# Optimization experiments

Measured on AMD Instinct MI355X. Metric: run time of the kernel, lower is better.

Reference implementation:

```python
import jax, jax.numpy as jnp
import numpy as np

B, S, E, M = 128, 196, 768, 768

def setup_inputs() -> dict:
    key = jax.random.key(0)
    k1, k2, k3, k4, k5 = jax.random.split(key, 5)
    sent_emb = jax.random.normal(k1, (B, S, E), dtype=jnp.float32)
    # valid event spans: start in [0, S-6), end = start + len, len in [1,5]
    starts = jax.random.randint(k2, (B, 2), 0, S - 6)
    lens = jax.random.randint(k3, (B, 2), 1, 6)
    ends = starts + lens
    batch_e = jnp.stack([starts[:, 0], ends[:, 0], starts[:, 1], ends[:, 1]], axis=1).astype(jnp.int64)
    mlp_w = jax.random.normal(k4, (M, 2 * E), dtype=jnp.float32) * 0.02
    mlp_b = jnp.zeros((M,), dtype=jnp.float32)
    fk_w = jax.random.normal(k5, (M, S * E), dtype=jnp.float32) * 0.005
    fk_b = jnp.zeros((M,), dtype=jnp.float32)
    return {"sent_emb": sent_emb, "batch_e": batch_e, "mlp_w": mlp_w,
            "mlp_b": mlp_b, "fk_w": fk_w, "fk_b": fk_b, "batch_size": B}

def reference(sent_emb, batch_e, mlp_w, mlp_b, fk_w, fk_b, batch_size):
    b, s, e = sent_emb.shape
    # sent_process: flatten each sentence's [S,E] embeddings into one row [S*E]
    sent_emb_cat = sent_emb.reshape(b, s * e)  # [B, S*E]
    # extract_event: mean-pool over the two variable-length spans (vectorized via masks)
    pos = jnp.arange(s)  # [S]
    m1 = ((pos >= batch_e[:, 0:1]) & (pos < batch_e[:, 1:2])).astype(sent_emb.dtype)  # [B,S]
    m2 = ((pos >= batch_e[:, 2:3]) & (pos < batch_e[:, 3:4])).astype(sent_emb.dtype)
    e1 = jnp.einsum('bs,bse->be', m1, sent_emb) / jnp.sum(m1, axis=1, keepdims=True)
    e2 = jnp.einsum('bs,bse->be', m2, sent_emb) / jnp.sum(m2, axis=1, keepdims=True)
    event_pair = jnp.concatenate([e1, e2], axis=1)  # [B, 2E]
    pred = 0.9 * (event_pair @ mlp_w.T + mlp_b) + 0.1 * (sent_emb_cat @ fk_w.T + fk_b)
    return pred
```

## Files before the change

kernel.cpp:

```cpp
#include <hip/hip_runtime.h>
#include <hip/hip_bf16.h>

#define B_ 128
#define S_ 196
#define E_ 768
#define M_ 768
#define KTOT (S_*E_)
#define BK 256
#define SS_TOTAL (KTOT/BK)
#define KSPLIT 32
#define BN 48
#define MTN (M_/BN)
#define PITCH 528
#define ZC 4

typedef __bf16 bf16x8 __attribute__((ext_vector_type(8)));
typedef __bf16 bf16x4 __attribute__((ext_vector_type(4)));
typedef float  f32x4  __attribute__((ext_vector_type(4)));

__device__ inline bf16x8 cvt8(const float* __restrict__ p) {
    float4 a = *(const float4*)p;
    float4 b = *(const float4*)(p + 4);
    bf16x8 r;
    r[0] = (__bf16)a.x; r[1] = (__bf16)a.y; r[2] = (__bf16)a.z; r[3] = (__bf16)a.w;
    r[4] = (__bf16)b.x; r[5] = (__bf16)b.y; r[6] = (__bf16)b.z; r[7] = (__bf16)b.w;
    return r;
}

__device__ inline void barrier_nodrain() {
    asm volatile("s_waitcnt lgkmcnt(0)" ::: "memory");
    __builtin_amdgcn_s_barrier();
}

__global__ void prep(const float* __restrict__ mlp_b,
                     const float* __restrict__ fk_b,
                     const float* __restrict__ A,
                     const int* __restrict__ BE, int be_stride,
                     float* __restrict__ out,
                     float* __restrict__ EP,
                     __bf16* __restrict__ Apk) {
    const int bid = blockIdx.x;
    if (bid < 384) {
        int i = bid * 256 + threadIdx.x;
        int m = i % M_;
        out[i] = 0.9f * mlp_b[m] + 0.1f * fk_b[m];
    } else if (bid < 512) {
        int b = bid - 384;
        int s1 = BE[(b*4 + 0) * be_stride];
        int e1 = BE[(b*4 + 1) * be_stride];
        int s2 = BE[(b*4 + 2) * be_stride];
        int e2 = BE[(b*4 + 3) * be_stride];
        float inv1 = 1.0f / (float)(e1 - s1);
        float inv2 = 1.0f / (float)(e2 - s2);
        for (int c = threadIdx.x; c < E_; c += 256) {
            float sum1 = 0.f, sum2 = 0.f;
            for (int s = s1; s < e1; ++s) sum1 += A[((size_t)b * S_ + s) * E_ + c];
            for (int s = s2; s < e2; ++s) sum2 += A[((size_t)b * S_ + s) * E_ + c];
            EP[b * (2*E_) + c]       = sum1 * inv1;
            EP[b * (2*E_) + E_ + c]  = sum2 * inv2;
        }
    } else {
        const int nchunk = SS_TOTAL * 8 * 8 * 64;
        for (int c = (bid - 512) * 256 + threadIdx.x; c < nchunk; c += 3072 * 256) {
            int lane = c & 63;
            int kf   = (c >> 6) & 7;
            int bt   = (c >> 9) & 7;
            int ss   = c >> 12;
            int b = bt * 16 + (lane & 15);
            int k = ss * BK + kf * 32 + (lane >> 4) * 8;
            *(bf16x8*)(Apk + (size_t)c * 8) = cvt8(A + (size_t)b * KTOT + k);
        }
    }
}


#define LOAD_A(AREG, sl)                                                      \
    _Pragma("unroll")                                                         \
    for (int kf = 0; kf < 8; ++kf)                                            \
        AREG[kf] = *(const bf16x8*)(abase + (size_t)(sl) * 32768 + kf * 512);

#define LOAD_W(sl)                                                            \
    _Pragma("unroll")                                                         \
    for (int i = 0; i < 6; ++i)                                               \
        w[i] = *(const float4*)(wbase + (size_t)i * KTOT + (size_t)(sl) * BK);

#define WRITE_W(buf)                                                          \
    _Pragma("unroll")                                                         \
    for (int i = 0; i < 6; ++i) {                                             \
        bf16x4 h;                                                             \
        h[0] = (__bf16)w[i].x; h[1] = (__bf16)w[i].y;                         \
        h[2] = (__bf16)w[i].z; h[3] = (__bf16)w[i].w;                         \
        *(bf16x4*)(&Wlds[buf][0] + wb + i * PITCH) = h;                       \
    }

#define COMPUTE(AREG, buf)                                                    \
    _Pragma("unroll")                                                         \
    for (int kf = 0; kf < 8; ++kf) {                                          \
        _Pragma("unroll")                                                     \
        for (int n = 0; n < 3; ++n) {                                         \
            bf16x8 wf = *(const bf16x8*)(&Wlds[buf][0] +                      \
                        (n * 16 + r16) * PITCH + kf * 64 + kg * 16);          \
            acc[n] = __builtin_amdgcn_mfma_f32_16x16x32_bf16(AREG[kf], wf,    \
                                                             acc[n], 0, 0, 0);\
        }                                                                     \
    }

__global__
__attribute__((amdgpu_flat_work_group_size(512, 512), amdgpu_waves_per_eu(4, 4)))
void fk_gemm(const __bf16* __restrict__ Apk,
             const float* __restrict__ W,
             float* __restrict__ partial) {
    __shared__ __align__(16) char Wlds[2][BN * PITCH];

    const int wg   = blockIdx.x;
    const int xcd  = wg & 7;
    const int slot = wg >> 3;
    const int kz   = (slot >> 4) * 8 + xcd;
    const int mt   = slot & 15;
    const int ss0 = (SS_TOTAL * kz) / KSPLIT;
    const int SSN = (SS_TOTAL * (kz + 1)) / KSPLIT - ss0;

    const int tid = threadIdx.x;
    const int wv  = tid >> 6;
    const int lane = tid & 63;
    const int r16 = lane & 15;
    const int kg  = lane >> 4;

    const float*  wbase = W + (size_t)(mt * BN + wv * 6) * KTOT
                            + (size_t)ss0 * BK + lane * 4;
    const int     wb    = (wv * 6) * PITCH + lane * 8;
    const __bf16* abase = Apk + ((size_t)ss0 * 8 + wv) * 4096 + lane * 8;

    f32x4 acc[3] = {};
    float4 w[6];
    bf16x8 aA[8], aB[8];

    LOAD_W(0)
    WRITE_W(0)
    LOAD_A(aA, 0)
    LOAD_W(1)
    barrier_nodrain();

    int sl = 0;
    for (; sl + 1 < SSN; sl += 2) {
        LOAD_A(aB, sl + 1)
        COMPUTE(aA, 0)
        WRITE_W(1)
        const bool more2 = (sl + 2 < SSN);
        if (more2) { LOAD_W(sl + 2) }
        barrier_nodrain();
        if (more2) { LOAD_A(aA, sl + 2) }
        COMPUTE(aB, 1)
        if (more2) {
            WRITE_W(0)
            if (sl + 3 < SSN) { LOAD_W(sl + 3) }
            barrier_nodrain();
        }
    }
    if (SSN & 1) {
        COMPUTE(aA, 0)
    }

    float* pz = partial + (size_t)kz * (B_ * M_);
#pragma unroll
    for (int n = 0; n < 3; ++n) {
        const int m = mt * BN + n * 16 + r16;
#pragma unroll
        for (int r = 0; r < 4; ++r) {
            const int b = wv * 16 + kg * 4 + r;
            pz[(size_t)b * M_ + m] = acc[n][r];
        }
    }
}

__global__ __launch_bounds__(256) void post(const float* __restrict__ pp,
                                            const float* __restrict__ EP,
                                            const float* __restrict__ Wm,
                                            float* __restrict__ out) {
    const int bid = blockIdx.x;
    if (bid < 1536) {
        int t = bid * 256 + threadIdx.x;
        int i = t % (B_ * M_);
        int zc = t / (B_ * M_);
        float s = 0.f;
#pragma unroll
        for (int z = zc * (KSPLIT / ZC); z < (zc + 1) * (KSPLIT / ZC); ++z)
            s += pp[(size_t)z * (B_ * M_) + i];
        atomicAdd(out + i, 0.1f * s);
    } else {
        const int wid   = ((bid - 1536) * 256 + threadIdx.x) >> 6;
        const int lane  = threadIdx.x & 63;
        const int bt    = wid & 7;
        const int mt    = wid >> 3;
        const int row16 = lane & 15;
        const int kgrp  = lane >> 4;
        const float* Arow = EP + (size_t)(bt*16 + row16) * (2*E_);
        const float* Brow = Wm + (size_t)(mt*16 + row16) * (2*E_);
        f32x4 acc = {};
        for (int k0 = 0; k0 < 2*E_; k0 += 32) {
            bf16x8 af = cvt8(Arow + k0 + kgrp*8);
            bf16x8 bv = cvt8(Brow + k0 + kgrp*8);
            acc = __builtin_amdgcn_mfma_f32_16x16x32_bf16(af, bv, acc, 0, 0, 0);
        }
        const int m = mt*16 + row16;
#pragma unroll
        for (int r = 0; r < 4; ++r) {
            const int b = bt*16 + kgrp*4 + r;
            atomicAdd(out + b * M_ + m, 0.9f * acc[r]);
        }
    }
}

extern "C" void kernel_launch(void* const* d_in, const int* in_sizes, int n_in,
                              void* d_out, int out_size, void* d_ws, size_t ws_size,
                              hipStream_t stream) {
    const float* se    = (const float*)d_in[0];
    const int*   be    = (const int*)  d_in[1];
    const float* mlp_w = (const float*)d_in[2];
    const float* mlp_b = (const float*)d_in[3];
    const float* fk_w  = (const float*)d_in[4];
    const float* fk_b  = (const float*)d_in[5];
    float* out = (float*)d_out;
    float* ep  = (float*)d_ws;
    float* pp  = ep + (size_t)B_ * 2 * E_;
    __bf16* apk = (__bf16*)(pp + (size_t)KSPLIT * B_ * M_);

    const int be_stride = (in_sizes[1] == B_ * 4 * 2) ? 2 : 1;

    prep<<<3584, 256, 0, stream>>>(mlp_b, fk_b, se, be, be_stride, out, ep, apk);
    fk_gemm<<<MTN * KSPLIT, 512, 0, stream>>>(apk, fk_w, pp);
    post<<<1632, 256, 0, stream>>>(pp, ep, mlp_w, out);
}
```

Baseline: 167.3 us.

## Restructure fk_gemm pipeline to prefetch W two slices ahead and single-buffer A

Reorganizes the main GEMM loop so each iteration prefetches the next pair of W slices into two register sets while computing both LDS buffers. The A fragment is loaded immediately before each compute instead of being double-buffered in registers. This reduces A register pressure and gives W loads a full pair of iterations of latency hiding. The cost is exposed A global-load latency right before the MFMAs, plus two barriers per pair instead of interleaved single barriers.

Measured after the change: 177.1 us. +5.9%, slower.

```diff
diff --git a/kernel.cpp b/kernel.cpp
--- a/kernel.cpp
+++ b/kernel.cpp
@@ -74,33 +74,40 @@
 }
 
 
-#define LOAD_A(AREG, sl)                                                      \
+#define LOAD_A(sl)                                                            \
     _Pragma("unroll")                                                         \
     for (int kf = 0; kf < 8; ++kf)                                            \
-        AREG[kf] = *(const bf16x8*)(abase + (size_t)(sl) * 32768 + kf * 512);
-
-#define LOAD_W(sl)                                                            \
+        aA[kf] = *(const bf16x8*)(abase + (size_t)(sl) * 32768 + kf * 512);
+
+#define LOAD_PAIR(sl)                                                         \
+    _Pragma("unroll")                                                         \
+    for (int i = 0; i < 6; ++i) {                                             \
+        w0[i] = *(const float4*)(wbase + (size_t)i * KTOT + (size_t)(sl) * BK);\
+        w1[i] = *(const float4*)(wbase + (size_t)i * KTOT + (size_t)(sl) * BK + BK);\
+    }
+
+#define LOAD_ONE(WREG, sl)                                                    \
     _Pragma("unroll")                                                         \
     for (int i = 0; i < 6; ++i)                                               \
-        w[i] = *(const float4*)(wbase + (size_t)i * KTOT + (size_t)(sl) * BK);
-
-#define WRITE_W(buf)                                                          \
+        WREG[i] = *(const float4*)(wbase + (size_t)i * KTOT + (size_t)(sl) * BK);
+
+#define WRITE_W(WREG, buf)                                                    \
     _Pragma("unroll")                                                         \
     for (int i = 0; i < 6; ++i) {                                             \
         bf16x4 h;                                                             \
-        h[0] = (__bf16)w[i].x; h[1] = (__bf16)w[i].y;                         \
-        h[2] = (__bf16)w[i].z; h[3] = (__bf16)w[i].w;                         \
+        h[0] = (__bf16)WREG[i].x; h[1] = (__bf16)WREG[i].y;                   \
+        h[2] = (__bf16)WREG[i].z; h[3] = (__bf16)WREG[i].w;                   \
         *(bf16x4*)(&Wlds[buf][0] + wb + i * PITCH) = h;                       \
     }
 
-#define COMPUTE(AREG, buf)                                                    \
+#define COMPUTE(buf)                                                          \
     _Pragma("unroll")                                                         \
     for (int kf = 0; kf < 8; ++kf) {                                          \
         _Pragma("unroll")                                                     \
         for (int n = 0; n < 3; ++n) {                                         \
             bf16x8 wf = *(const bf16x8*)(&Wlds[buf][0] +                      \
                         (n * 16 + r16) * PITCH + kf * 64 + kg * 16);          \
-            acc[n] = __builtin_amdgcn_mfma_f32_16x16x32_bf16(AREG[kf], wf,    \
+            acc[n] = __builtin_amdgcn_mfma_f32_16x16x32_bf16(aA[kf], wf,      \
                                                              acc[n], 0, 0, 0);\
         }                                                                     \
     }
@@ -132,33 +139,31 @@
     const __bf16* abase = Apk + ((size_t)ss0 * 8 + wv) * 4096 + lane * 8;
 
     f32x4 acc[3] = {};
-    float4 w[6];
-    bf16x8 aA[8], aB[8];
-
-    LOAD_W(0)
-    WRITE_W(0)
-    LOAD_A(aA, 0)
-    LOAD_W(1)
+    float4 w0[6], w1[6];
+    bf16x8 aA[8];
+
+    LOAD_PAIR(0)
+    WRITE_W(w0, 0)
+    WRITE_W(w1, 1)
     barrier_nodrain();
 
-    int sl = 0;
-    for (; sl + 1 < SSN; sl += 2) {
-        LOAD_A(aB, sl + 1)
-        COMPUTE(aA, 0)
-        WRITE_W(1)
-        const bool more2 = (sl + 2 < SSN);
-        if (more2) { LOAD_W(sl + 2) }
+    const int P = SSN >> 1;
+    for (int p = 0; p < P; ++p) {
+        const int nxt = 2 * p + 2;
+        if (nxt + 1 < SSN)      { LOAD_PAIR(nxt) }
+        else if (nxt < SSN)     { LOAD_ONE(w0, nxt) }
+        LOAD_A(2 * p)
+        COMPUTE(0)
+        LOAD_A(2 * p + 1)
+        COMPUTE(1)
         barrier_nodrain();
-        if (more2) { LOAD_A(aA, sl + 2) }
-        COMPUTE(aB, 1)
-        if (more2) {
-            WRITE_W(0)
-            if (sl + 3 < SSN) { LOAD_W(sl + 3) }
-            barrier_nodrain();
-        }
+        if (nxt < SSN)          { WRITE_W(w0, 0) }
+        if (nxt + 1 < SSN)      { WRITE_W(w1, 1) }
+        barrier_nodrain();
     }
     if (SSN & 1) {
-        COMPUTE(aA, 0)
+        LOAD_A(SSN - 1)
+        COMPUTE(0)
     }
 
     float* pz = partial + (size_t)kz * (B_ * M_);
```
